# Kernel tuning notes

Measured on AMD Instinct MI355X. Metric: run time of the kernel, lower is better.

The kernel has to match this reference:

```python
import jax, jax.numpy as jnp
import numpy as np

B, L, DIM, H, HD = 1, 2048, 2048, 16, 128  # head_dim = DIM // H; RoPE pairs = HD // 2


def setup_inputs() -> dict:
    key = jax.random.key(0)
    ks = jax.random.split(key, 6)
    x = jax.random.normal(ks[0], (B, L, DIM), dtype=jnp.float32)
    pe = jax.random.normal(ks[1], (1, 1, L, HD // 2, 2, 2), dtype=jnp.float32)
    qkv_w = jax.random.normal(ks[2], (3 * DIM, DIM), dtype=jnp.float32) * 0.02
    q_scale = jnp.ones((HD,), dtype=jnp.float32)
    k_scale = jnp.ones((HD,), dtype=jnp.float32)
    proj_w = jax.random.normal(ks[3], (DIM, DIM), dtype=jnp.float32) * 0.02
    proj_b = jnp.zeros((DIM,), dtype=jnp.float32)
    return {"x": x, "pe": pe, "qkv_w": qkv_w, "q_scale": q_scale,
            "k_scale": k_scale, "proj_w": proj_w, "proj_b": proj_b}


def _rmsnorm(t, scale):
    # per-head-dim RMSNorm, eps=1e-6, computed in fp32 (inputs already fp32)
    rrms = jax.lax.rsqrt(jnp.mean(t * t, axis=-1, keepdims=True) + 1e-6)
    return t * rrms * scale


def _apply_rope(q, k, pe):
    def rot(t):
        t_ = t.reshape(*t.shape[:-1], -1, 1, 2)  # [B,H,L,HD/2,1,2]
        out = pe[..., 0] * t_[..., 0] + pe[..., 1] * t_[..., 1]  # [B,H,L,HD/2,2]
        return out.reshape(t.shape)
    return rot(q), rot(k)


def reference(x, pe, qkv_w, q_scale, k_scale, proj_w, proj_b):
    b, l, _ = x.shape
    qkv = jnp.einsum('bld,ed->ble', x, qkv_w)  # [B, L, 3*DIM]
    qkv = qkv.reshape(b, l, 3, H, HD)
    # 'B L (K H D) -> K B H L D'
    qkv = jnp.transpose(qkv, (2, 0, 3, 1, 4))
    q, k, v = qkv[0], qkv[1], qkv[2]  # each [B, H, L, HD]
    q = _rmsnorm(q, q_scale)
    k = _rmsnorm(k, k_scale)
    q, k = _apply_rope(q, k, pe)
    scale = 1.0 / jnp.sqrt(jnp.asarray(HD, dtype=q.dtype))
    scores = jnp.einsum('bhqd,bhkd->bhqk', q, k) * scale
    attn = jax.nn.softmax(scores, axis=-1)
    out = jnp.einsum('bhqk,bhkd->bhqd', attn, v)  # [B, H, L, HD]
    out = jnp.transpose(out, (0, 2, 1, 3)).reshape(b, l, H * HD)  # 'B H L D -> B L (H D)'
    return jnp.einsum('bld,ed->ble', out, proj_w) + proj_b
```

## Files before the change

kernel.cpp:

```cpp
#include <hip/hip_runtime.h>
#include <hip/hip_bf16.h>
#include <math.h>

#define L_SEQ 2048
#define DIM   2048
#define NH    16
#define HD    128
#define TDIM  6144

typedef __attribute__((ext_vector_type(8))) short short8;
typedef __attribute__((ext_vector_type(4))) float f32x4;
typedef __attribute__((ext_vector_type(4))) unsigned int u32x4;

__device__ __forceinline__ void gl_lds16(const void* g, void* l) {
  __builtin_amdgcn_global_load_lds(
      (const __attribute__((address_space(1))) unsigned int*)g,
      (__attribute__((address_space(3))) unsigned int*)l, 16, 0, 0);
}

__device__ __forceinline__ short bf16bits(float x) {
  __hip_bfloat16 h = __float2bfloat16(x);
  return *(short*)&h;
}

__device__ __forceinline__ float bits2f(short s) {
  unsigned int u = ((unsigned int)(unsigned short)s) << 16;
  return __uint_as_float(u);
}

__device__ __forceinline__ unsigned int pack_bf16(float a, float b) {
  __hip_bfloat162 h = __float22bfloat162_rn(make_float2(a, b));
  return *(unsigned int*)&h;
}

__global__ __launch_bounds__(256)
void cast2_bf16(const float* __restrict__ a, __hip_bfloat16* __restrict__ oa,
                const float* __restrict__ b, __hip_bfloat16* __restrict__ ob) {
  int i = (blockIdx.x * 256 + threadIdx.x) * 8;
  const float* src;
  __hip_bfloat16* dst;
  int off;
  if (i < DIM * DIM) { src = a; dst = oa; off = i; }
  else               { src = b; dst = ob; off = i - DIM * DIM; }
  float4 v0 = *(const float4*)(src + off);
  float4 v1 = *(const float4*)(src + off + 4);
  short8 o;
  o[0] = bf16bits(v0.x); o[1] = bf16bits(v0.y); o[2] = bf16bits(v0.z); o[3] = bf16bits(v0.w);
  o[4] = bf16bits(v1.x); o[5] = bf16bits(v1.y); o[6] = bf16bits(v1.z); o[7] = bf16bits(v1.w);
  *(short8*)(dst + off) = o;
}

__global__ __launch_bounds__(256)
void cast_bf16(const float* __restrict__ in, __hip_bfloat16* __restrict__ out, int n) {
  int i = (blockIdx.x * 256 + threadIdx.x) * 8;
  if (i >= n) return;
  float4 a = *(const float4*)(in + i);
  float4 b = *(const float4*)(in + i + 4);
  short8 o;
  o[0] = bf16bits(a.x); o[1] = bf16bits(a.y); o[2] = bf16bits(a.z); o[3] = bf16bits(a.w);
  o[4] = bf16bits(b.x); o[5] = bf16bits(b.y); o[6] = bf16bits(b.z); o[7] = bf16bits(b.w);
  *(short8*)(out + i) = o;
}

__global__ __launch_bounds__(256)
void gemm_qkv_fused(const __hip_bfloat16* __restrict__ A, const __hip_bfloat16* __restrict__ B,
                    const float* __restrict__ q_scale, const float* __restrict__ k_scale,
                    const float* __restrict__ pe,
                    __hip_bfloat16* __restrict__ Qb, __hip_bfloat16* __restrict__ Kb,
                    __hip_bfloat16* __restrict__ Vt) {
  const int K = DIM;
  const int bx = blockIdx.x;
  const int n0 = bx * 128, m0 = blockIdx.y * 128;
  const int t = threadIdx.x, lane = t & 63, w = t >> 6;
  const int l15 = lane & 15, quad = lane >> 4;
  const int wm = (w & 1) * 64, wn = (w >> 1) * 64;

  __shared__ __align__(16) char smem[128 * 136 * 2];
  __hip_bfloat16* As = (__hip_bfloat16*)smem;
  __hip_bfloat16* Bs = As + 128 * 32;

  f32x4 acc[4][4];
#pragma unroll
  for (int mt = 0; mt < 4; ++mt)
#pragma unroll
    for (int nt = 0; nt < 4; ++nt) acc[mt][nt] = (f32x4){0.f, 0.f, 0.f, 0.f};

  const int arow  = lane >> 2;
  const int acol8 = (lane & 3) * 8;
  const __hip_bfloat16* Ab = A + (size_t)(m0 + w * 16 + arow) * K + acol8;
  const __hip_bfloat16* Bb = B + (size_t)(n0 + w * 16 + arow) * K + acol8;
  __hip_bfloat16* As_base = As + (size_t)(w * 16) * 32;
  __hip_bfloat16* Bs_base = Bs + (size_t)(w * 16) * 32;

  for (int kb = 0; kb < K; kb += 32) {
    gl_lds16(Ab + kb,                As_base);
    gl_lds16(Ab + kb + (size_t)64*K, As_base + 64 * 32);
    gl_lds16(Bb + kb,                Bs_base);
    gl_lds16(Bb + kb + (size_t)64*K, Bs_base + 64 * 32);
    __syncthreads();

    short8 am[4], bn[4];
#pragma unroll
    for (int mt = 0; mt < 4; ++mt)
      am[mt] = *(const short8*)&As[(size_t)(wm + mt*16 + l15) * 32 + quad * 8];
#pragma unroll
    for (int nt = 0; nt < 4; ++nt)
      bn[nt] = *(const short8*)&Bs[(size_t)(wn + nt*16 + l15) * 32 + quad * 8];
#pragma unroll
    for (int mt = 0; mt < 4; ++mt)
#pragma unroll
      for (int nt = 0; nt < 4; ++nt)
        acc[mt][nt] = __builtin_amdgcn_mfma_f32_16x16x32_bf16(am[mt], bn[nt], acc[mt][nt], 0, 0, 0);
    __syncthreads();
  }

  __hip_bfloat16* T = (__hip_bfloat16*)smem;

  if (bx < 32) {
    const float* scale = (bx < 16) ? q_scale : k_scale;
    const float qmul = (bx < 16) ? 0.08838834764831845f : 1.0f;
    __hip_bfloat16* dst = (bx < 16) ? Qb : Kb;
    const int h = bx & 15;

#pragma unroll
    for (int mt = 0; mt < 4; ++mt)
#pragma unroll
      for (int nt = 0; nt < 4; ++nt) {
        int d = wn + nt * 16 + l15;
#pragma unroll
        for (int r = 0; r < 4; ++r)
          T[(wm + mt * 16 + quad * 4 + r) * 136 + d] = __float2bfloat16(acc[mt][nt][r]);
      }
    __syncthreads();

    const int row  = t >> 1;
    const int half = t & 1;
    const __hip_bfloat16* Trow = T + row * 136 + half * 64;

    float ss = 0.f;
#pragma unroll
    for (int c8 = 0; c8 < 64; c8 += 8) {
      short8 v8 = *(const short8*)(Trow + c8);
#pragma unroll
      for (int j = 0; j < 8; ++j) { float f = bits2f(v8[j]); ss += f * f; }
    }
    ss += __shfl_xor(ss, 1);
    const float rrms = rsqrtf(ss * (1.f / 128.f) + 1e-6f);

    const int l = m0 + row;
    const float* perow = pe + (size_t)l * 256 + half * 128;
    __hip_bfloat16* drow = dst + ((size_t)h * L_SEQ + l) * HD + half * 64;

#pragma unroll
    for (int c8 = 0; c8 < 64; c8 += 8) {
      short8 v8 = *(const short8*)(Trow + c8);
      float f[8];
#pragma unroll
      for (int j = 0; j < 8; ++j)
        f[j] = bits2f(v8[j]) * rrms * scale[half * 64 + c8 + j];
      short8 o;
#pragma unroll
      for (int p = 0; p < 4; ++p) {
        float4 pp = *(const float4*)(perow + c8 * 2 + p * 4);
        float e = f[2 * p], od = f[2 * p + 1];
        o[2 * p]     = bf16bits((pp.x * e + pp.y * od) * qmul);
        o[2 * p + 1] = bf16bits((pp.z * e + pp.w * od) * qmul);
      }
      *(short8*)(drow + c8) = o;
    }
  } else {
    const int h = bx - 32;
#pragma unroll
    for (int mt = 0; mt < 4; ++mt)
#pragma unroll
      for (int nt = 0; nt < 4; ++nt) {
        int d = wn + nt * 16 + l15;
#pragma unroll
        for (int r = 0; r < 4; ++r) {
          int l_local = wm + mt * 16 + quad * 4 + r;
          T[d * 136 + l_local] = __float2bfloat16(acc[mt][nt][r]);
        }
      }
    __syncthreads();
#pragma unroll
    for (int it = 0; it < 8; ++it) {
      int idx = t + it * 256;
      int d = idx >> 4, c8 = (idx & 15) * 8;
      short8 v = *(const short8*)&T[d * 136 + c8];
      *(short8*)&Vt[((size_t)h * HD + d) * L_SEQ + m0 + c8] = v;
    }
  }
}

__global__ __launch_bounds__(256)
void gemm_proj(const __hip_bfloat16* __restrict__ A, const __hip_bfloat16* __restrict__ B,
               const float* __restrict__ bias, float* __restrict__ C,
               int M, int N, int K) {
  const int n0 = blockIdx.x * 128, m0 = blockIdx.y * 128;
  const int t = threadIdx.x, lane = t & 63, w = t >> 6;
  const int l15 = lane & 15, quad = lane >> 4;
  const int wm = (w & 1) * 64, wn = (w >> 1) * 64;

  __shared__ __align__(16) __hip_bfloat16 As[128 * 32];
  __shared__ __align__(16) __hip_bfloat16 Bs[128 * 32];

  f32x4 acc[4][4];
#pragma unroll
  for (int mt = 0; mt < 4; ++mt)
#pragma unroll
    for (int nt = 0; nt < 4; ++nt) acc[mt][nt] = (f32x4){0.f, 0.f, 0.f, 0.f};

  const int arow  = lane >> 2;
  const int acol8 = (lane & 3) * 8;
  const __hip_bfloat16* Ab = A + (size_t)(m0 + w * 16 + arow) * K + acol8;
  const __hip_bfloat16* Bb = B + (size_t)(n0 + w * 16 + arow) * K + acol8;
  __hip_bfloat16* As_base = As + (size_t)(w * 16) * 32;
  __hip_bfloat16* Bs_base = Bs + (size_t)(w * 16) * 32;

  for (int kb = 0; kb < K; kb += 32) {
    gl_lds16(Ab + kb,                As_base);
    gl_lds16(Ab + kb + (size_t)64*K, As_base + 64 * 32);
    gl_lds16(Bb + kb,                Bs_base);
    gl_lds16(Bb + kb + (size_t)64*K, Bs_base + 64 * 32);
    __syncthreads();

    short8 am[4], bn[4];
#pragma unroll
    for (int mt = 0; mt < 4; ++mt)
      am[mt] = *(const short8*)&As[(size_t)(wm + mt*16 + l15) * 32 + quad * 8];
#pragma unroll
    for (int nt = 0; nt < 4; ++nt)
      bn[nt] = *(const short8*)&Bs[(size_t)(wn + nt*16 + l15) * 32 + quad * 8];
#pragma unroll
    for (int mt = 0; mt < 4; ++mt)
#pragma unroll
      for (int nt = 0; nt < 4; ++nt)
        acc[mt][nt] = __builtin_amdgcn_mfma_f32_16x16x32_bf16(am[mt], bn[nt], acc[mt][nt], 0, 0, 0);
    __syncthreads();
  }

#pragma unroll
  for (int mt = 0; mt < 4; ++mt)
#pragma unroll
    for (int nt = 0; nt < 4; ++nt) {
      int col = n0 + wn + nt * 16 + l15;
#pragma unroll
      for (int r = 0; r < 4; ++r) {
        int row = m0 + wm + mt * 16 + quad * 4 + r;
        C[(size_t)row * N + col] = acc[mt][nt][r] + bias[col];
      }
    }
}

__global__ __launch_bounds__(256, 4)
void attn_mfma(const __hip_bfloat16* __restrict__ Qb,
               const __hip_bfloat16* __restrict__ Kb,
               const __hip_bfloat16* __restrict__ Vt,
               __hip_bfloat16* __restrict__ Opart, float2* __restrict__ ml) {
  const int q0 = blockIdx.x * 64;
  const int h  = blockIdx.y;
  const int z  = blockIdx.z;
  const int t  = threadIdx.x;
  const int lane = t & 63, w = t >> 6;
  const int l15 = lane & 15, quad = lane >> 4;
  const int sw = l15 & 7;

  __shared__ __align__(16) __hip_bfloat16 Ks[64 * 128];
  __shared__ __align__(16) __hip_bfloat16 Vs[128 * 64];

  const __hip_bfloat16* kbase = Kb + (size_t)h * L_SEQ * HD;
  const __hip_bfloat16* vbase = Vt + (size_t)h * HD * L_SEQ;

  short8 aq[4];
  {
    const __hip_bfloat16* qbase = Qb + ((size_t)h * L_SEQ + q0 + w * 16 + l15) * HD;
#pragma unroll
    for (int ks = 0; ks < 4; ++ks)
      aq[ks] = *(const short8*)(qbase + ks * 32 + quad * 8);
  }

  f32x4 o[8];
#pragma unroll
  for (int n2 = 0; n2 < 8; ++n2) o[n2] = (f32x4){0.f, 0.f, 0.f, 0.f};
  float m_run = -1e30f, l_run = 0.f;

  for (int kt = 0; kt < 16; ++kt) {
    const int k0 = z * (L_SEQ / 2) + kt * 64;
#pragma unroll
    for (int i = 0; i < 4; ++i) {
      int krow = w * 16 + i * 4 + (lane >> 4);
      int kch  = (lane & 15) ^ (krow & 7);
      gl_lds16(kbase + (size_t)(k0 + krow) * HD + kch * 8,
               &Ks[(w * 16 + i * 4) * 128]);
    }
#pragma unroll
    for (int i = 0; i < 4; ++i) {
      int vrow = w * 32 + i * 8 + (lane >> 3);
      int vch  = (lane & 7) ^ (vrow & 7);
      gl_lds16(vbase + (size_t)vrow * L_SEQ + k0 + vch * 8,
               &Vs[(w * 32 + i * 8) * 64]);
    }
    __syncthreads();

    f32x4 s[4];
#pragma unroll
    for (int nt = 0; nt < 4; ++nt) s[nt] = (f32x4){0.f, 0.f, 0.f, 0.f};
#pragma unroll
    for (int ks = 0; ks < 4; ++ks) {
      short8 bk[4];
#pragma unroll
      for (int nt = 0; nt < 4; ++nt)
        bk[nt] = *(const short8*)&Ks[(nt * 16 + l15) * 128 + ((ks * 4 + quad) ^ sw) * 8];
#pragma unroll
      for (int nt = 0; nt < 4; ++nt)
        s[nt] = __builtin_amdgcn_mfma_f32_16x16x32_bf16(bk[nt], aq[ks], s[nt], 0, 0, 0);
    }

    float mx0 = fmaxf(fmaxf(s[0][0], s[0][1]), fmaxf(s[0][2], s[0][3]));
    float mx1 = fmaxf(fmaxf(s[1][0], s[1][1]), fmaxf(s[1][2], s[1][3]));
    float mx2 = fmaxf(fmaxf(s[2][0], s[2][1]), fmaxf(s[2][2], s[2][3]));
    float mx3 = fmaxf(fmaxf(s[3][0], s[3][1]), fmaxf(s[3][2], s[3][3]));
    float rm = fmaxf(fmaxf(mx0, mx1), fmaxf(mx2, mx3));
    rm = fmaxf(rm, __shfl_xor(rm, 16));
    rm = fmaxf(rm, __shfl_xor(rm, 32));
    float mnew = fmaxf(m_run, rm);
    float alpha = __expf(m_run - mnew);
    m_run = mnew;

    float sum = 0.f;
#pragma unroll
    for (int nt = 0; nt < 4; ++nt)
#pragma unroll
      for (int r = 0; r < 4; ++r) {
        float p = __expf(s[nt][r] - mnew);
        s[nt][r] = p;
        sum += p;
      }
    sum += __shfl_xor(sum, 16);
    sum += __shfl_xor(sum, 32);
    l_run = l_run * alpha + sum;

    float alpha_r[4];
#pragma unroll
    for (int r = 0; r < 4; ++r) alpha_r[r] = __shfl(alpha, quad * 4 + r);
#pragma unroll
    for (int n2 = 0; n2 < 8; ++n2)
#pragma unroll
      for (int r = 0; r < 4; ++r) o[n2][r] *= alpha_r[r];

    unsigned int pk[4][2];
#pragma unroll
    for (int nt = 0; nt < 4; ++nt) {
      pk[nt][0] = pack_bf16(s[nt][0], s[nt][1]);
      pk[nt][1] = pack_bf16(s[nt][2], s[nt][3]);
    }
    short8 ap[2];
#pragma unroll
    for (int ks2 = 0; ks2 < 2; ++ks2) {
      u32x4 a32;
#pragma unroll
      for (int jp = 0; jp < 4; ++jp) {
        int quad_src = (quad & 1) * 2 + (jp >> 1);
        int src = (quad_src << 4) | l15;
        int rp = jp & 1;
        unsigned int v0 = __shfl((int)pk[2 * ks2 + 0][rp], src);
        unsigned int v1 = __shfl((int)pk[2 * ks2 + 1][rp], src);
        a32[jp] = (quad >> 1) ? v1 : v0;
      }
      ap[ks2] = *(short8*)&a32;
    }

#pragma unroll
    for (int ks2 = 0; ks2 < 2; ++ks2)
#pragma unroll
      for (int n2 = 0; n2 < 8; ++n2) {
        short8 bv = *(const short8*)&Vs[(n2 * 16 + l15) * 64 + ((ks2 * 4 + quad) ^ sw) * 8];
        o[n2] = __builtin_amdgcn_mfma_f32_16x16x32_bf16(ap[ks2], bv, o[n2], 0, 0, 0);
      }

    __syncthreads();
  }

  const size_t rb = (size_t)(z * NH + h) * L_SEQ + q0 + w * 16;
  float linv[4];
#pragma unroll
  for (int r = 0; r < 4; ++r) linv[r] = 1.f / __shfl(l_run, quad * 4 + r);
#pragma unroll
  for (int r = 0; r < 4; ++r) {
    size_t row = rb + quad * 4 + r;
#pragma unroll
    for (int n2 = 0; n2 < 8; ++n2)
      Opart[row * HD + n2 * 16 + l15] = __float2bfloat16(o[n2][r] * linv[r]);
  }
  if (quad == 0) ml[rb + l15] = make_float2(m_run, l_run);
}

__global__ __launch_bounds__(256)
void attn_combine(const __hip_bfloat16* __restrict__ Opart,
                  const float2* __restrict__ ml,
                  __hip_bfloat16* __restrict__ out) {
  const int h  = blockIdx.y;
  const int q  = blockIdx.x * 16 + (threadIdx.x >> 4);
  const int d8 = (threadIdx.x & 15) * 8;
  const size_t i0 = (size_t)h * L_SEQ + q;
  const size_t i1 = (size_t)(NH + h) * L_SEQ + q;
  float2 a = ml[i0], b = ml[i1];
  float M  = fmaxf(a.x, b.x);
  float w1 = __expf(a.x - M) * a.y;
  float w2 = __expf(b.x - M) * b.y;
  float inv = 1.f / (w1 + w2);
  w1 *= inv; w2 *= inv;
  short8 o1 = *(const short8*)&Opart[i0 * HD + d8];
  short8 o2 = *(const short8*)&Opart[i1 * HD + d8];
  short8 r;
#pragma unroll
  for (int j = 0; j < 8; ++j)
    r[j] = bf16bits(w1 * bits2f(o1[j]) + w2 * bits2f(o2[j]));
  *(short8*)&out[(size_t)q * DIM + h * HD + d8] = r;
}

extern "C" void kernel_launch(void* const* d_in, const int* in_sizes, int n_in,
                              void* d_out, int out_size, void* d_ws, size_t ws_size,
                              hipStream_t stream) {
  const float* x       = (const float*)d_in[0];
  const float* pe      = (const float*)d_in[1];
  const float* qkv_w   = (const float*)d_in[2];
  const float* q_scale = (const float*)d_in[3];
  const float* k_scale = (const float*)d_in[4];
  const float* proj_w  = (const float*)d_in[5];
  const float* proj_b  = (const float*)d_in[6];
  float* out = (float*)d_out;

  char* base = (char*)d_ws;
  __hip_bfloat16* xb       = (__hip_bfloat16*)base;
  __hip_bfloat16* wb       = (__hip_bfloat16*)(base + 8388608);
  __hip_bfloat16* Qb       = (__hip_bfloat16*)(base + 33554432);
  __hip_bfloat16* Kb       = (__hip_bfloat16*)(base + 41943040);
  __hip_bfloat16* Vt       = (__hip_bfloat16*)(base + 50331648);
  __hip_bfloat16* pwb      = (__hip_bfloat16*)(base + 58720256);
  __hip_bfloat16* Opart    = (__hip_bfloat16*)(base + 8388608);
  float2*         ml       = (float2*)(base + 25165824);
  __hip_bfloat16* attn_out = (__hip_bfloat16*)base;

  cast2_bf16<<<dim3((DIM * DIM + TDIM * DIM) / (256 * 8)), 256, 0, stream>>>(
      x, xb, qkv_w, wb);

  gemm_qkv_fused<<<dim3(TDIM / 128, L_SEQ / 128), 256, 0, stream>>>(
      xb, wb, q_scale, k_scale, pe, Qb, Kb, Vt);

  cast_bf16<<<dim3(DIM * DIM / (256 * 8)), 256, 0, stream>>>(proj_w, pwb, DIM * DIM);

  attn_mfma<<<dim3(L_SEQ / 64, NH, 2), 256, 0, stream>>>(Qb, Kb, Vt, Opart, ml);
  attn_combine<<<dim3(L_SEQ / 16, NH), 256, 0, stream>>>(Opart, ml, attn_out);

  gemm_proj<<<dim3(DIM / 128, DIM / 128), 256, 0, stream>>>(
      attn_out, pwb, proj_b, out, L_SEQ, DIM, DIM);
}
```

Before: 341.3 us.

## Split QKV projection into pipelined 256x256 GEMM and separate epilogue kernel

```diff
diff --git a/kernel.cpp b/kernel.cpp
--- a/kernel.cpp
+++ b/kernel.cpp
@@ -62,98 +62,142 @@
   *(short8*)(out + i) = o;
 }
 
+#define QKV_N 6144
+#define QKV_K 2048
+
+__global__ __launch_bounds__(512, 2)
+void gemm_qkv_256(const __hip_bfloat16* __restrict__ A,
+                  const __hip_bfloat16* __restrict__ B,
+                  __hip_bfloat16* __restrict__ C) {
+  extern __shared__ char smem[];
+  const int tid  = threadIdx.x;
+  const int lane = tid & 63, w = tid >> 6;
+  const int l15  = lane & 15, quad = lane >> 4;
+  const int wm   = w >> 2, wn = w & 3;
+
+  const int orig = blockIdx.x;
+  const int by = orig & 7;
+  const int bx = orig >> 3;
+  const int m0 = by * 256, n0 = bx * 256;
+
+  const int ar0 = tid >> 2,         aq0 = tid & 3;
+  const int ar1 = (512 + tid) >> 2, aq1 = (512 + tid) & 3;
+  const __hip_bfloat16* pA0 = A + (size_t)(m0 + ar0) * QKV_K + aq0 * 8;
+  const __hip_bfloat16* pA1 = A + (size_t)(m0 + ar1) * QKV_K + aq1 * 8;
+  const __hip_bfloat16* pB0 = B + (size_t)(n0 + ar0) * QKV_K + aq0 * 8;
+  const __hip_bfloat16* pB1 = B + (size_t)(n0 + ar1) * QKV_K + aq1 * 8;
+  const int dst0 = w * 1024;
+
+  f32x4 acc[8][4];
+#pragma unroll
+  for (int mi = 0; mi < 8; ++mi)
+#pragma unroll
+    for (int ni = 0; ni < 4; ++ni) acc[mi][ni] = (f32x4){0.f, 0.f, 0.f, 0.f};
+
+  const int aoff = ((wm * 128 + l15) * 32 + quad * 8) * 2;
+  const int boff = ((wn * 64 + l15) * 32 + quad * 8) * 2;
+
+#pragma unroll
+  for (int p = 0; p < 3; ++p) {
+    char* Sp = smem + p * 32768;
+    gl_lds16(pA0 + p * 32, Sp + dst0);
+    gl_lds16(pA1 + p * 32, Sp + dst0 + 8192);
+    gl_lds16(pB0 + p * 32, Sp + 16384 + dst0);
+    gl_lds16(pB1 + p * 32, Sp + 16384 + dst0 + 8192);
+  }
+  asm volatile("s_waitcnt vmcnt(8)\n\ts_barrier" ::: "memory");
+
+  for (int tb = 0; tb < 64; tb += 4) {
+#pragma unroll
+    for (int u = 0; u < 4; ++u) {
+      const int t  = tb + u;
+      const char* As = smem + u * 32768;
+      const char* Bs = As + 16384;
+      const int tn = (t + 3) & 63;
+      char* Sn = smem + ((u + 3) & 3) * 32768;
+
+      short8 a[8];
+#pragma unroll
+      for (int mi = 0; mi < 8; ++mi)
+        a[mi] = *(const short8*)(As + aoff + mi * 1024);
+      short8 b0 = *(const short8*)(Bs + boff);
+      short8 b1 = *(const short8*)(Bs + boff + 1024);
+      gl_lds16(pA0 + tn * 32, Sn + dst0);
+      gl_lds16(pA1 + tn * 32, Sn + dst0 + 8192);
+      __builtin_amdgcn_s_barrier();
+      __builtin_amdgcn_s_setprio(1);
+#pragma unroll
+      for (int mi = 0; mi < 8; ++mi) {
+        acc[mi][0] = __builtin_amdgcn_mfma_f32_16x16x32_bf16(a[mi], b0, acc[mi][0], 0, 0, 0);
+        acc[mi][1] = __builtin_amdgcn_mfma_f32_16x16x32_bf16(a[mi], b1, acc[mi][1], 0, 0, 0);
+      }
+      __builtin_amdgcn_s_setprio(0);
+      __builtin_amdgcn_s_barrier();
+
+      short8 b2 = *(const short8*)(Bs + boff + 2048);
+      short8 b3 = *(const short8*)(Bs + boff + 3072);
+      gl_lds16(pB0 + tn * 32, Sn + 16384 + dst0);
+      gl_lds16(pB1 + tn * 32, Sn + 16384 + dst0 + 8192);
+      asm volatile("s_waitcnt vmcnt(8)\n\ts_barrier" ::: "memory");
+      __builtin_amdgcn_s_setprio(1);
+#pragma unroll
+      for (int mi = 0; mi < 8; ++mi) {
+        acc[mi][2] = __builtin_amdgcn_mfma_f32_16x16x32_bf16(a[mi], b2, acc[mi][2], 0, 0, 0);
+        acc[mi][3] = __builtin_amdgcn_mfma_f32_16x16x32_bf16(a[mi], b3, acc[mi][3], 0, 0, 0);
+      }
+      __builtin_amdgcn_s_setprio(0);
+      __builtin_amdgcn_s_barrier();
+    }
+  }
+
+  const int crow = m0 + wm * 128 + quad * 4;
+  const int ccol = n0 + wn * 64 + l15;
+#pragma unroll
+  for (int mi = 0; mi < 8; ++mi)
+#pragma unroll
+    for (int ni = 0; ni < 4; ++ni)
+#pragma unroll
+      for (int r = 0; r < 4; ++r)
+        C[(size_t)(crow + mi * 16 + r) * QKV_N + ccol + ni * 16] =
+            __float2bfloat16(acc[mi][ni][r]);
+}
+
 __global__ __launch_bounds__(256)
-void gemm_qkv_fused(const __hip_bfloat16* __restrict__ A, const __hip_bfloat16* __restrict__ B,
-                    const float* __restrict__ q_scale, const float* __restrict__ k_scale,
-                    const float* __restrict__ pe,
-                    __hip_bfloat16* __restrict__ Qb, __hip_bfloat16* __restrict__ Kb,
-                    __hip_bfloat16* __restrict__ Vt) {
-  const int K = DIM;
-  const int bx = blockIdx.x;
-  const int n0 = bx * 128, m0 = blockIdx.y * 128;
-  const int t = threadIdx.x, lane = t & 63, w = t >> 6;
-  const int l15 = lane & 15, quad = lane >> 4;
-  const int wm = (w & 1) * 64, wn = (w >> 1) * 64;
-
-  __shared__ __align__(16) char smem[128 * 136 * 2];
-  __hip_bfloat16* As = (__hip_bfloat16*)smem;
-  __hip_bfloat16* Bs = As + 128 * 32;
-
-  f32x4 acc[4][4];
-#pragma unroll
-  for (int mt = 0; mt < 4; ++mt)
-#pragma unroll
-    for (int nt = 0; nt < 4; ++nt) acc[mt][nt] = (f32x4){0.f, 0.f, 0.f, 0.f};
-
-  const int arow  = lane >> 2;
-  const int acol8 = (lane & 3) * 8;
-  const __hip_bfloat16* Ab = A + (size_t)(m0 + w * 16 + arow) * K + acol8;
-  const __hip_bfloat16* Bb = B + (size_t)(n0 + w * 16 + arow) * K + acol8;
-  __hip_bfloat16* As_base = As + (size_t)(w * 16) * 32;
-  __hip_bfloat16* Bs_base = Bs + (size_t)(w * 16) * 32;
-
-  for (int kb = 0; kb < K; kb += 32) {
-    gl_lds16(Ab + kb,                As_base);
-    gl_lds16(Ab + kb + (size_t)64*K, As_base + 64 * 32);
-    gl_lds16(Bb + kb,                Bs_base);
-    gl_lds16(Bb + kb + (size_t)64*K, Bs_base + 64 * 32);
-    __syncthreads();
-
-    short8 am[4], bn[4];
-#pragma unroll
-    for (int mt = 0; mt < 4; ++mt)
-      am[mt] = *(const short8*)&As[(size_t)(wm + mt*16 + l15) * 32 + quad * 8];
-#pragma unroll
-    for (int nt = 0; nt < 4; ++nt)
-      bn[nt] = *(const short8*)&Bs[(size_t)(wn + nt*16 + l15) * 32 + quad * 8];
-#pragma unroll
-    for (int mt = 0; mt < 4; ++mt)
-#pragma unroll
-      for (int nt = 0; nt < 4; ++nt)
-        acc[mt][nt] = __builtin_amdgcn_mfma_f32_16x16x32_bf16(am[mt], bn[nt], acc[mt][nt], 0, 0, 0);
-    __syncthreads();
-  }
-
-  __hip_bfloat16* T = (__hip_bfloat16*)smem;
-
-  if (bx < 32) {
-    const float* scale = (bx < 16) ? q_scale : k_scale;
-    const float qmul = (bx < 16) ? 0.08838834764831845f : 1.0f;
-    __hip_bfloat16* dst = (bx < 16) ? Qb : Kb;
-    const int h = bx & 15;
-
-#pragma unroll
-    for (int mt = 0; mt < 4; ++mt)
-#pragma unroll
-      for (int nt = 0; nt < 4; ++nt) {
-        int d = wn + nt * 16 + l15;
-#pragma unroll
-        for (int r = 0; r < 4; ++r)
-          T[(wm + mt * 16 + quad * 4 + r) * 136 + d] = __float2bfloat16(acc[mt][nt][r]);
-      }
-    __syncthreads();
-
-    const int row  = t >> 1;
-    const int half = t & 1;
-    const __hip_bfloat16* Trow = T + row * 136 + half * 64;
+void qkv_epilogue(const __hip_bfloat16* __restrict__ C,
+                  const float* __restrict__ q_scale, const float* __restrict__ k_scale,
+                  const float* __restrict__ pe,
+                  __hip_bfloat16* __restrict__ Qb, __hip_bfloat16* __restrict__ Kb,
+                  __hip_bfloat16* __restrict__ Vt) {
+  const int bid = blockIdx.x;
+  const int t = threadIdx.x;
+  if (bid < 512) {
+    const int sec = bid >> 8;
+    const int h   = (bid >> 4) & 15;
+    const int rb  = bid & 15;
+    const float* scale = sec ? k_scale : q_scale;
+    const float qmul = sec ? 1.0f : 0.08838834764831845f;
+    __hip_bfloat16* dst = sec ? Kb : Qb;
+
+    const int row = t >> 1, half = t & 1;
+    const int l = rb * 128 + row;
+    const __hip_bfloat16* grow = C + (size_t)l * TDIM + sec * DIM + h * HD + half * 64;
 
     float ss = 0.f;
 #pragma unroll
     for (int c8 = 0; c8 < 64; c8 += 8) {
-      short8 v8 = *(const short8*)(Trow + c8);
+      short8 v8 = *(const short8*)(grow + c8);
 #pragma unroll
       for (int j = 0; j < 8; ++j) { float f = bits2f(v8[j]); ss += f * f; }
     }
     ss += __shfl_xor(ss, 1);
     const float rrms = rsqrtf(ss * (1.f / 128.f) + 1e-6f);
 
-    const int l = m0 + row;
     const float* perow = pe + (size_t)l * 256 + half * 128;
     __hip_bfloat16* drow = dst + ((size_t)h * L_SEQ + l) * HD + half * 64;
 
 #pragma unroll
     for (int c8 = 0; c8 < 64; c8 += 8) {
-      short8 v8 = *(const short8*)(Trow + c8);
+      short8 v8 = *(const short8*)(grow + c8);
       float f[8];
 #pragma unroll
       for (int j = 0; j < 8; ++j)
@@ -169,25 +213,25 @@
       *(short8*)(drow + c8) = o;
     }
   } else {
-    const int h = bx - 32;
-#pragma unroll
-    for (int mt = 0; mt < 4; ++mt)
-#pragma unroll
-      for (int nt = 0; nt < 4; ++nt) {
-        int d = wn + nt * 16 + l15;
-#pragma unroll
-        for (int r = 0; r < 4; ++r) {
-          int l_local = wm + mt * 16 + quad * 4 + r;
-          T[d * 136 + l_local] = __float2bfloat16(acc[mt][nt][r]);
-        }
-      }
+    __shared__ short Tt[128 * 72];
+    const int vb = bid - 512;
+    const int h = vb >> 5, lb = vb & 31;
+    const int l0 = lb * 64;
+#pragma unroll
+    for (int k = 0; k < 4; ++k) {
+      int idx = t + k * 256;
+      int row = idx >> 4, c = idx & 15;
+      short8 v = *(const short8*)(C + (size_t)(l0 + row) * TDIM + 2 * DIM + h * HD + c * 8);
+#pragma unroll
+      for (int j = 0; j < 8; ++j) Tt[(c * 8 + j) * 72 + row] = v[j];
+    }
     __syncthreads();
-#pragma unroll
-    for (int it = 0; it < 8; ++it) {
-      int idx = t + it * 256;
-      int d = idx >> 4, c8 = (idx & 15) * 8;
-      short8 v = *(const short8*)&T[d * 136 + c8];
-      *(short8*)&Vt[((size_t)h * HD + d) * L_SEQ + m0 + c8] = v;
+    const int d = t >> 1, lh = t & 1;
+    __hip_bfloat16* vrow = Vt + ((size_t)h * HD + d) * L_SEQ + l0 + lh * 32;
+#pragma unroll
+    for (int k = 0; k < 4; ++k) {
+      short8 o = *(const short8*)&Tt[d * 72 + lh * 32 + k * 8];
+      *(short8*)(vrow + k * 8) = o;
     }
   }
 }
@@ -434,19 +478,28 @@
   char* base = (char*)d_ws;
   __hip_bfloat16* xb       = (__hip_bfloat16*)base;
   __hip_bfloat16* wb       = (__hip_bfloat16*)(base + 8388608);
-  __hip_bfloat16* Qb       = (__hip_bfloat16*)(base + 33554432);
-  __hip_bfloat16* Kb       = (__hip_bfloat16*)(base + 41943040);
-  __hip_bfloat16* Vt       = (__hip_bfloat16*)(base + 50331648);
+  __hip_bfloat16* Cq       = (__hip_bfloat16*)(base + 33554432);
   __hip_bfloat16* pwb      = (__hip_bfloat16*)(base + 58720256);
-  __hip_bfloat16* Opart    = (__hip_bfloat16*)(base + 8388608);
-  float2*         ml       = (float2*)(base + 25165824);
-  __hip_bfloat16* attn_out = (__hip_bfloat16*)base;
+  __hip_bfloat16* Qb       = (__hip_bfloat16*)base;
+  __hip_bfloat16* Kb       = (__hip_bfloat16*)(base + 8388608);
+  __hip_bfloat16* Vt       = (__hip_bfloat16*)(base + 16777216);
+  __hip_bfloat16* Opart    = (__hip_bfloat16*)(base + 33554432);
+  float2*         ml       = (float2*)(base + 50331648);
+  __hip_bfloat16* attn_out = (__hip_bfloat16*)(base + 25165824);
+
+  static bool attr_done = false;
+  if (!attr_done) {
+    hipFuncSetAttribute((const void*)gemm_qkv_256,
+                        hipFuncAttributeMaxDynamicSharedMemorySize, 131072);
+    attr_done = true;
+  }
 
   cast2_bf16<<<dim3((DIM * DIM + TDIM * DIM) / (256 * 8)), 256, 0, stream>>>(
       x, xb, qkv_w, wb);
 
-  gemm_qkv_fused<<<dim3(TDIM / 128, L_SEQ / 128), 256, 0, stream>>>(
-      xb, wb, q_scale, k_scale, pe, Qb, Kb, Vt);
+  gemm_qkv_256<<<dim3((TDIM / 256) * (L_SEQ / 256)), 512, 131072, stream>>>(xb, wb, Cq);
+
+  qkv_epilogue<<<dim3(1024), 256, 0, stream>>>(Cq, q_scale, k_scale, pe, Qb, Kb, Vt);
 
   cast_bf16<<<dim3(DIM * DIM / (256 * 8)), 256, 0, stream>>>(proj_w, pwb, DIM * DIM);
 
```

After: 329.5 us. 3.5% less time.
